# Kernel optimization log

Measured on AMD Instinct MI355X. Metric: run time of the kernel, lower is better.

## Reference

```python
import jax, jax.numpy as jnp
import numpy as np

EMBED_DIM = 1280
NUM_HEADS = 16
HEAD_DIM = EMBED_DIM // NUM_HEADS  # 80
SCALE = HEAD_DIM ** -0.5
BATCH = 16
SEQ = 1024


def setup_inputs() -> dict:
    key = jax.random.key(0)
    k1, k2, k3, k4, k5 = jax.random.split(key, 5)
    return {
        "hidden_states": jax.random.normal(k1, (BATCH, SEQ, EMBED_DIM), dtype=jnp.float32),
        "w_qkv": jax.random.normal(k2, (EMBED_DIM, 3 * EMBED_DIM), dtype=jnp.float32) * (EMBED_DIM ** -0.5),
        "b_qkv": jax.random.normal(k3, (3 * EMBED_DIM,), dtype=jnp.float32) * 0.02,
        "w_proj": jax.random.normal(k4, (EMBED_DIM, EMBED_DIM), dtype=jnp.float32) * (EMBED_DIM ** -0.5),
        "b_proj": jax.random.normal(k5, (EMBED_DIM,), dtype=jnp.float32) * 0.02,
    }


def reference(hidden_states, w_qkv, b_qkv, w_proj, b_proj):
    b, s, e = hidden_states.shape
    # QKV projection: [b, s, 3e] -> [3, b, h, s, d]
    qkv = hidden_states @ w_qkv + b_qkv
    qkv = qkv.reshape(b, s, 3, NUM_HEADS, HEAD_DIM).transpose(2, 0, 3, 1, 4)
    q, k, v = qkv[0], qkv[1], qkv[2]
    # full attention matrix [b, h, s, s]
    attn = jnp.einsum("bhqd,bhkd->bhqk", q, k) * SCALE
    attn = jax.nn.softmax(attn, axis=-1)
    # dropout p=0.0 (eval): identity
    out = jnp.einsum("bhqk,bhkd->bhqd", attn, v)
    out = out.transpose(0, 2, 1, 3).reshape(b, s, e)
    return out @ w_proj + b_proj
```

## Files before the change

### kernel.cpp

```cpp
#include <hip/hip_runtime.h>

#define BATCH 16
#define SEQ   1024
#define EMBED 1280
#define NH    16
#define HD    80
#define HDP   96
#define NQKV  3840
#define MTOK  (BATCH*SEQ)
#define SCALE 0.11180339887498948f
#define LOG2E 1.4426950408889634f

#define SK_STRIDE 104
#define SV_STRIDE 72
#define SP_STRIDE 72

typedef _Float16 half8 __attribute__((ext_vector_type(8)));
typedef _Float16 half4 __attribute__((ext_vector_type(4)));
typedef float floatx4 __attribute__((ext_vector_type(4)));

#define GLD_TO_LDS(gp, lp)                                                        \
  __builtin_amdgcn_global_load_lds(                                               \
      (const __attribute__((address_space(1))) void*)(gp),                        \
      (__attribute__((address_space(3))) void*)(lp), 16, 0, 0)

__device__ __forceinline__ float rowmax16(float x) {
#define DPP_MAX(ctrl)                                                             \
  {                                                                               \
    float y = __int_as_float(                                                     \
        __builtin_amdgcn_update_dpp(0, __float_as_int(x), ctrl, 0xF, 0xF, true)); \
    x = fmaxf(x, y);                                                              \
  }
  DPP_MAX(0xB1);
  DPP_MAX(0x4E);
  DPP_MAX(0x141);
  DPP_MAX(0x140);
#undef DPP_MAX
  return x;
}

__global__ void cvt_f32_to_f16(const float4* __restrict__ in, _Float16* __restrict__ out, int n4) {
  int i = blockIdx.x * blockDim.x + threadIdx.x;
  if (i < n4) {
    float4 v = in[i];
    half4 h;
    h[0] = (_Float16)v.x; h[1] = (_Float16)v.y; h[2] = (_Float16)v.z; h[3] = (_Float16)v.w;
    *(half4*)(out + (size_t)i * 4) = h;
  }
}

template <int N>
__global__ void cvt_transpose_f16(const float* __restrict__ in, _Float16* __restrict__ out) {
  __shared__ float tile[32][33];
  const int tx = threadIdx.x & 31, ty = threadIdx.x >> 5;
  const int k0 = blockIdx.y * 32;
  const int n0 = blockIdx.x * 32;
#pragma unroll
  for (int j = 0; j < 4; ++j)
    tile[ty + 8 * j][tx] = in[(size_t)(k0 + ty + 8 * j) * N + n0 + tx];
  __syncthreads();
#pragma unroll
  for (int j = 0; j < 4; ++j)
    out[(size_t)(n0 + ty + 8 * j) * 1280 + k0 + tx] = (_Float16)tile[tx][ty + 8 * j];
}

template <int MODE, int NT>
__global__ __launch_bounds__(256, 2)
void gemm_kernel(const _Float16* __restrict__ A, const _Float16* __restrict__ Bt,
                 const float* __restrict__ bias,
                 _Float16* __restrict__ q_pad, _Float16* __restrict__ k_pad,
                 _Float16* __restrict__ v_t, float* __restrict__ outf) {
  __shared__ __align__(16) _Float16 sA[2][128 * 32];
  __shared__ __align__(16) _Float16 sB[2][128 * 32];
  const int K = 1280;
  const int tid = threadIdx.x;
  const int wave = tid >> 6;
  const int lane = tid & 63;
  const int quad = lane >> 4;
  const int r16 = lane & 15;
  const int wm = wave >> 1, wn = wave & 1;

  const int pid = blockIdx.x;
  const int xcd = pid & 7;
  const int local = pid >> 3;
  const int panel = local / (8 * NT);
  const int rr = local - panel * (8 * NT);
  const int pm = rr & 7;
  const int pn = rr >> 3;
  const int m0 = (xcd * 16 + panel * 8 + pm) * 128;
  const int n0 = pn * 128;

  floatx4 acc[4][4] = {};

  const int c_base = wave * 128 + lane;

#define ISSUE(k0, buf)                                                              \
  do {                                                                              \
    _Pragma("unroll")                                                               \
    for (int i = 0; i < 2; ++i) {                                                   \
      int c = c_base + i * 64;                                                      \
      int row = c >> 2, kc = c & 3;                                                 \
      GLD_TO_LDS(A + (size_t)(m0 + row) * K + (k0) + kc * 8,                        \
                 &sA[buf][(wave * 2 + i) * 512]);                                   \
      GLD_TO_LDS(Bt + (size_t)(n0 + row) * K + (k0) + kc * 8,                       \
                 &sB[buf][(wave * 2 + i) * 512]);                                   \
    }                                                                               \
  } while (0)

  ISSUE(0, 0);
  for (int kt = 0; kt < 40; ++kt) {
    __syncthreads();
    if (kt + 1 < 40) ISSUE((kt + 1) * 32, (kt + 1) & 1);
    const _Float16* pA = sA[kt & 1];
    const _Float16* pB = sB[kt & 1];

    half8 af[4], bf[4];
#pragma unroll
    for (int mi = 0; mi < 4; ++mi)
      af[mi] = *(const half8*)(pA + (wm * 64 + mi * 16 + r16) * 32 + quad * 8);
#pragma unroll
    for (int ni = 0; ni < 4; ++ni)
      bf[ni] = *(const half8*)(pB + (wn * 64 + ni * 16 + r16) * 32 + quad * 8);
#pragma unroll
    for (int mi = 0; mi < 4; ++mi)
#pragma unroll
      for (int ni = 0; ni < 4; ++ni)
        acc[mi][ni] = __builtin_amdgcn_mfma_f32_16x16x32_f16(af[mi], bf[ni], acc[mi][ni], 0, 0, 0);
  }

  if (MODE == 1) {
#pragma unroll
    for (int mi = 0; mi < 4; ++mi)
#pragma unroll
      for (int ni = 0; ni < 4; ++ni) {
        int n = n0 + wn * 64 + ni * 16 + r16;
        float bv = bias[n];
#pragma unroll
        for (int r = 0; r < 4; ++r) {
          int m = m0 + wm * 64 + mi * 16 + quad * 4 + r;
          outf[(size_t)m * EMBED + n] = acc[mi][ni][r] + bv;
        }
      }
  } else {
#pragma unroll
    for (int mi = 0; mi < 4; ++mi)
#pragma unroll
      for (int ni = 0; ni < 4; ++ni) {
        int n = n0 + wn * 64 + ni * 16 + r16;
        float bv = bias[n];
        int which = n / 1280;
        int rem = n - which * 1280;
        int h = rem / 80;
        int d = rem - h * 80;
#pragma unroll
        for (int r = 0; r < 4; ++r) {
          int m = m0 + wm * 64 + mi * 16 + quad * 4 + r;
          int b = m >> 10, s = m & 1023;
          int bh = b * NH + h;
          _Float16 val = (_Float16)(acc[mi][ni][r] + bv);
          if (which == 0) {
            q_pad[((size_t)bh * SEQ + s) * HDP + d] = val;
            if (d < 16) q_pad[((size_t)bh * SEQ + s) * HDP + 80 + d] = (_Float16)0.f;
          } else if (which == 1) {
            k_pad[((size_t)bh * SEQ + s) * HDP + d] = val;
            if (d < 16) k_pad[((size_t)bh * SEQ + s) * HDP + 80 + d] = (_Float16)0.f;
          } else {
            v_t[((size_t)bh * HD + d) * SEQ + s] = val;
          }
        }
      }
  }
}

__global__ __launch_bounds__(256, 2)
void attn_kernel(const _Float16* __restrict__ q_pad, const _Float16* __restrict__ k_pad,
                 const _Float16* __restrict__ v_t, _Float16* __restrict__ attn_out) {
  __shared__ __align__(16) _Float16 sK[64 * SK_STRIDE];
  __shared__ __align__(16) _Float16 sV[96 * SV_STRIDE];
  __shared__ __align__(16) _Float16 sP[4][16 * SP_STRIDE];

  const int tid = threadIdx.x;
  const int wave = tid >> 6, lane = tid & 63, quad = lane >> 4, r16 = lane & 15;
  const int bh = blockIdx.x >> 3;
  const int q0 = (blockIdx.x & 7) * 128;

  if (tid < 128) {
    int row = 80 + (tid >> 3), col = (tid & 7) * 8;
    half8 z;
#pragma unroll
    for (int j = 0; j < 8; ++j) z[j] = (row == 80) ? (_Float16)1.f : (_Float16)0.f;
    *(half8*)(sV + row * SV_STRIDE + col) = z;
  }

  half8 qf[2][3];
#pragma unroll
  for (int mi = 0; mi < 2; ++mi) {
    const _Float16* qb = q_pad + ((size_t)bh * SEQ + q0 + wave * 32 + mi * 16 + r16) * HDP;
#pragma unroll
    for (int kq = 0; kq < 3; ++kq) {
      half8 q = *(const half8*)(qb + kq * 32 + quad * 8);
#pragma unroll
      for (int j = 0; j < 8; ++j) q[j] = q[j] * (_Float16)(SCALE * LOG2E);
      qf[mi][kq] = q;
    }
  }

  int rowK[3], colK[3];
#pragma unroll
  for (int i = 0; i < 3; ++i) {
    int c = tid + i * 256;
    rowK[i] = c / 12; colK[i] = c - rowK[i] * 12;
  }
  const int rowV0 = tid >> 3, colV0 = tid & 7;
  const _Float16* kgb = k_pad + ((size_t)bh * SEQ) * HDP;
  const _Float16* vgb = v_t + (size_t)bh * HD * SEQ;

  floatx4 o[2][6] = {};
  float mrow[2][4];
#pragma unroll
  for (int mi = 0; mi < 2; ++mi)
#pragma unroll
    for (int r = 0; r < 4; ++r) mrow[mi][r] = -1e30f;

  for (int kt = 0; kt < 16; ++kt) {
    __syncthreads();
    {
      uint4 tk0 = *(const uint4*)(kgb + ((size_t)(kt * 64 + rowK[0])) * HDP + colK[0] * 8);
      uint4 tk1 = *(const uint4*)(kgb + ((size_t)(kt * 64 + rowK[1])) * HDP + colK[1] * 8);
      uint4 tk2 = *(const uint4*)(kgb + ((size_t)(kt * 64 + rowK[2])) * HDP + colK[2] * 8);
      uint4 tv0 = *(const uint4*)(vgb + (size_t)(rowV0) * SEQ + kt * 64 + colV0 * 8);
      uint4 tv1 = *(const uint4*)(vgb + (size_t)(rowV0 + 32) * SEQ + kt * 64 + colV0 * 8);
      uint4 tv2;
      if (tid < 128)
        tv2 = *(const uint4*)(vgb + (size_t)(rowV0 + 64) * SEQ + kt * 64 + colV0 * 8);
      *(uint4*)(sK + rowK[0] * SK_STRIDE + colK[0] * 8) = tk0;
      *(uint4*)(sK + rowK[1] * SK_STRIDE + colK[1] * 8) = tk1;
      *(uint4*)(sK + rowK[2] * SK_STRIDE + colK[2] * 8) = tk2;
      *(uint4*)(sV + (rowV0) * SV_STRIDE + colV0 * 8) = tv0;
      *(uint4*)(sV + (rowV0 + 32) * SV_STRIDE + colV0 * 8) = tv1;
      if (tid < 128)
        *(uint4*)(sV + (rowV0 + 64) * SV_STRIDE + colV0 * 8) = tv2;
    }
    __syncthreads();

    floatx4 sacc[2][4] = {};
#pragma unroll
    for (int ni = 0; ni < 4; ++ni)
#pragma unroll
      for (int kq = 0; kq < 3; ++kq) {
        half8 kf = *(const half8*)(sK + (ni * 16 + r16) * SK_STRIDE + kq * 32 + quad * 8);
#pragma unroll
        for (int mi = 0; mi < 2; ++mi)
          sacc[mi][ni] = __builtin_amdgcn_mfma_f32_16x16x32_f16(qf[mi][kq], kf, sacc[mi][ni], 0, 0, 0);
      }

#pragma unroll
    for (int mi = 0; mi < 2; ++mi)
#pragma unroll
      for (int r = 0; r < 4; ++r) {
        float mx = fmaxf(fmaxf(sacc[mi][0][r], sacc[mi][1][r]),
                         fmaxf(sacc[mi][2][r], sacc[mi][3][r]));
        mx = rowmax16(mx);
        float mnew = fmaxf(mrow[mi][r], mx);
        float alpha = __builtin_amdgcn_exp2f(mrow[mi][r] - mnew);
        mrow[mi][r] = mnew;
#pragma unroll
        for (int ni = 0; ni < 4; ++ni)
          sacc[mi][ni][r] = __builtin_amdgcn_exp2f(sacc[mi][ni][r] - mnew);
#pragma unroll
        for (int di = 0; di < 6; ++di) o[mi][di][r] *= alpha;
      }

#pragma unroll
    for (int mi = 0; mi < 2; ++mi) {
#pragma unroll
      for (int ni = 0; ni < 4; ++ni)
#pragma unroll
        for (int r = 0; r < 4; ++r)
          sP[wave][(quad * 4 + r) * SP_STRIDE + ni * 16 + r16] = (_Float16)sacc[mi][ni][r];
#pragma unroll
      for (int kp = 0; kp < 2; ++kp) {
        half8 pf = *(const half8*)(&sP[wave][r16 * SP_STRIDE + kp * 32 + quad * 8]);
#pragma unroll
        for (int di = 0; di < 6; ++di) {
          half8 vf = *(const half8*)(sV + (di * 16 + r16) * SV_STRIDE + kp * 32 + quad * 8);
          o[mi][di] = __builtin_amdgcn_mfma_f32_16x16x32_f16(pf, vf, o[mi][di], 0, 0, 0);
        }
      }
    }
  }

  const int b = bh >> 4, h = bh & 15;
#pragma unroll
  for (int mi = 0; mi < 2; ++mi)
#pragma unroll
    for (int r = 0; r < 4; ++r) {
      float l = __shfl(o[mi][5][r], lane & 48);
      float inv = 1.0f / l;
      int tok = b * SEQ + q0 + wave * 32 + mi * 16 + quad * 4 + r;
#pragma unroll
      for (int di = 0; di < 5; ++di) {
        int e = h * HD + di * 16 + r16;
        attn_out[(size_t)tok * EMBED + e] = (_Float16)(o[mi][di][r] * inv);
      }
    }
}

extern "C" void kernel_launch(void* const* d_in, const int* in_sizes, int n_in,
                              void* d_out, int out_size, void* d_ws, size_t ws_size,
                              hipStream_t stream) {
  const float* hidden = (const float*)d_in[0];
  const float* w_qkv  = (const float*)d_in[1];
  const float* b_qkv  = (const float*)d_in[2];
  const float* w_proj = (const float*)d_in[3];
  const float* b_proj = (const float*)d_in[4];
  float* out = (float*)d_out;

  char* ws = (char*)d_ws;
  size_t off = 0;
  _Float16* hidden_h = (_Float16*)(ws + off); off += (size_t)MTOK * EMBED * 2;
  _Float16* wqkv_t   = (_Float16*)(ws + off); off += (size_t)NQKV * EMBED * 2;
  _Float16* wproj_t  = (_Float16*)(ws + off); off += (size_t)EMBED * EMBED * 2;
  _Float16* q_pad    = (_Float16*)(ws + off); off += (size_t)BATCH * NH * SEQ * HDP * 2;
  _Float16* k_pad    = (_Float16*)(ws + off); off += (size_t)BATCH * NH * SEQ * HDP * 2;
  _Float16* v_t      = (_Float16*)(ws + off); off += (size_t)BATCH * NH * HD * SEQ * 2;
  _Float16* attn_out = hidden_h;

  {
    int n4 = MTOK * EMBED / 4;
    cvt_f32_to_f16<<<(n4 + 255) / 256, 256, 0, stream>>>((const float4*)hidden, hidden_h, n4);
  }
  cvt_transpose_f16<NQKV><<<dim3(NQKV / 32, 1280 / 32), 256, 0, stream>>>(w_qkv, wqkv_t);
  cvt_transpose_f16<EMBED><<<dim3(EMBED / 32, 1280 / 32), 256, 0, stream>>>(w_proj, wproj_t);

  gemm_kernel<0, 30><<<128 * 30, 256, 0, stream>>>(
      hidden_h, wqkv_t, b_qkv, q_pad, k_pad, v_t, nullptr);

  attn_kernel<<<BATCH * NH * (SEQ / 128), 256, 0, stream>>>(q_pad, k_pad, v_t, attn_out);

  gemm_kernel<1, 10><<<128 * 10, 256, 0, stream>>>(
      attn_out, wproj_t, b_proj, nullptr, nullptr, nullptr, out);
}
```

Before: 677.8 us.

## Replace 128x128 GEMM with 256x256 8-wave pipelined GEMM with swizzled LDS

Both projection GEMMs move from a 128x128x32 tile with 4 waves to a 256x256x64 tile with 8 waves. Loads are staged in half-tiles and interleaved with MFMA quadrants under explicit barriers, s_setprio and vmcnt waits. The LDS layout uses an XOR swizzle to avoid bank conflicts. The larger tile raises data reuse per LDS byte, but it also increases LDS use (128KB) and register pressure, and it relies on hand-tuned waitcnt correctness.

```diff
diff --git a/kernel.cpp b/kernel.cpp
--- a/kernel.cpp
+++ b/kernel.cpp
@@ -64,86 +64,139 @@
     out[(size_t)(n0 + ty + 8 * j) * 1280 + k0 + tx] = (_Float16)tile[tx][ty + 8 * j];
 }
 
-template <int MODE, int NT>
-__global__ __launch_bounds__(256, 2)
-void gemm_kernel(const _Float16* __restrict__ A, const _Float16* __restrict__ Bt,
-                 const float* __restrict__ bias,
-                 _Float16* __restrict__ q_pad, _Float16* __restrict__ k_pad,
-                 _Float16* __restrict__ v_t, float* __restrict__ outf) {
-  __shared__ __align__(16) _Float16 sA[2][128 * 32];
-  __shared__ __align__(16) _Float16 sB[2][128 * 32];
-  const int K = 1280;
+
+#define STAGE_A(H, T, D)                                                           \
+  do {                                                                             \
+    GLD_TO_LDS(aSrc0 + (size_t)((H) * 128) * 1280 + (T) * 64,                      \
+               &sA[D][((H) * 128 + wave * 16) * 64]);                              \
+    GLD_TO_LDS(aSrc0 + (size_t)((H) * 128 + 8) * 1280 + (T) * 64,                  \
+               &sA[D][((H) * 128 + wave * 16 + 8) * 64]);                          \
+  } while (0)
+
+#define STAGE_B(H, T, D)                                                           \
+  do {                                                                             \
+    GLD_TO_LDS(bSrc0 + (size_t)((H) * 128) * 1280 + (T) * 64,                      \
+               &sB[D][((H) * 128 + wave * 16) * 64]);                              \
+    GLD_TO_LDS(bSrc0 + (size_t)((H) * 128 + 8) * 1280 + (T) * 64,                  \
+               &sB[D][((H) * 128 + wave * 16 + 8) * 64]);                          \
+  } while (0)
+
+#define LDS_FRAG(P, ROWB, FR, KK) (*(const half8*)((P) + ((ROWB) + (FR) * 16) * 64 + cofs[KK]))
+
+#define MFMA_Q(MIB, NIB)                                                           \
+  _Pragma("unroll") for (int mi = 0; mi < 4; ++mi)                                 \
+    _Pragma("unroll") for (int ni = 0; ni < 2; ++ni)                               \
+      _Pragma("unroll") for (int kk = 0; kk < 2; ++kk)                             \
+        acc[(MIB) + mi][(NIB) + ni] = __builtin_amdgcn_mfma_f32_16x16x32_f16(      \
+            af[mi][kk], bf[(NIB) + ni][kk], acc[(MIB) + mi][(NIB) + ni], 0, 0, 0)
+
+#define GBODY(T, D, S1, S2, VNSTR)                                                 \
+  {                                                                                \
+    const _Float16* pA = &sA[D][0];                                                \
+    const _Float16* pB = &sB[D][0];                                                \
+                         \
+    _Pragma("unroll") for (int mi = 0; mi < 4; ++mi)                               \
+      _Pragma("unroll") for (int kk = 0; kk < 2; ++kk)                             \
+        af[mi][kk] = LDS_FRAG(pA, rA, mi, kk);                                     \
+    _Pragma("unroll") for (int ni = 0; ni < 2; ++ni)                               \
+      _Pragma("unroll") for (int kk = 0; kk < 2; ++kk)                             \
+        bf[ni][kk] = LDS_FRAG(pB, rB, ni, kk);                                     \
+    if (S1) { STAGE_A(1, (T) + 1, (D) ^ 1); }                                      \
+    __builtin_amdgcn_s_barrier();                                                  \
+    asm volatile("s_waitcnt lgkmcnt(0)" ::: "memory");                             \
+    __builtin_amdgcn_s_setprio(1);                                                 \
+    MFMA_Q(0, 0);                                                                  \
+    __builtin_amdgcn_s_setprio(0);                                                 \
+    __builtin_amdgcn_s_barrier();                                                  \
+                                                   \
+    _Pragma("unroll") for (int ni = 0; ni < 2; ++ni)                               \
+      _Pragma("unroll") for (int kk = 0; kk < 2; ++kk)                             \
+        bf[2 + ni][kk] = LDS_FRAG(pB, rB, 2 + ni, kk);                             \
+    __builtin_amdgcn_s_barrier();                                                  \
+    asm volatile("s_waitcnt lgkmcnt(0)" ::: "memory");                             \
+    __builtin_amdgcn_s_setprio(1);                                                 \
+    MFMA_Q(0, 2);                                                                  \
+    __builtin_amdgcn_s_setprio(0);                                                 \
+    __builtin_amdgcn_s_barrier();                                                  \
+                                  \
+    _Pragma("unroll") for (int mi = 0; mi < 4; ++mi)                               \
+      _Pragma("unroll") for (int kk = 0; kk < 2; ++kk)                             \
+        af[mi][kk] = LDS_FRAG(pA, rA, 4 + mi, kk);                                 \
+    if (S2) { STAGE_B(0, (T) + 2, (D)); }                                          \
+    __builtin_amdgcn_s_barrier();                                                  \
+    asm volatile("s_waitcnt lgkmcnt(0)" ::: "memory");                             \
+    __builtin_amdgcn_s_setprio(1);                                                 \
+    MFMA_Q(4, 0);                                                                  \
+    __builtin_amdgcn_s_setprio(0);                                                 \
+    __builtin_amdgcn_s_barrier();                                                  \
+            \
+    if (S2) { STAGE_A(0, (T) + 2, (D)); STAGE_B(1, (T) + 2, (D)); }                \
+    __builtin_amdgcn_s_barrier();                                                  \
+    __builtin_amdgcn_s_setprio(1);                                                 \
+    MFMA_Q(4, 2);                                                                  \
+    __builtin_amdgcn_s_setprio(0);                                                 \
+    asm volatile("s_waitcnt " VNSTR ::: "memory");                                 \
+    __builtin_amdgcn_s_barrier();                                                  \
+  }
+
+template <int MODE>
+__global__ __launch_bounds__(512, 2)
+void gemm256(const _Float16* __restrict__ A, const _Float16* __restrict__ Bt,
+             const float* __restrict__ bias,
+             _Float16* __restrict__ q_pad, _Float16* __restrict__ k_pad,
+             _Float16* __restrict__ v_t, float* __restrict__ outf) {
+  __shared__ __align__(16) _Float16 sA[2][256 * 64];
+  __shared__ __align__(16) _Float16 sB[2][256 * 64];
+
   const int tid = threadIdx.x;
-  const int wave = tid >> 6;
-  const int lane = tid & 63;
-  const int quad = lane >> 4;
-  const int r16 = lane & 15;
-  const int wm = wave >> 1, wn = wave & 1;
+  const int wave = tid >> 6, lane = tid & 63, quad = lane >> 4, r16 = lane & 15;
+  const int wm = wave >> 2, wn = wave & 3;
 
   const int pid = blockIdx.x;
-  const int xcd = pid & 7;
-  const int local = pid >> 3;
-  const int panel = local / (8 * NT);
-  const int rr = local - panel * (8 * NT);
-  const int pm = rr & 7;
-  const int pn = rr >> 3;
-  const int m0 = (xcd * 16 + panel * 8 + pm) * 128;
-  const int n0 = pn * 128;
-
-  floatx4 acc[4][4] = {};
-
-  const int c_base = wave * 128 + lane;
-
-#define ISSUE(k0, buf)                                                              \
-  do {                                                                              \
-    _Pragma("unroll")                                                               \
-    for (int i = 0; i < 2; ++i) {                                                   \
-      int c = c_base + i * 64;                                                      \
-      int row = c >> 2, kc = c & 3;                                                 \
-      GLD_TO_LDS(A + (size_t)(m0 + row) * K + (k0) + kc * 8,                        \
-                 &sA[buf][(wave * 2 + i) * 512]);                                   \
-      GLD_TO_LDS(Bt + (size_t)(n0 + row) * K + (k0) + kc * 8,                       \
-                 &sB[buf][(wave * 2 + i) * 512]);                                   \
-    }                                                                               \
-  } while (0)
-
-  ISSUE(0, 0);
-  for (int kt = 0; kt < 40; ++kt) {
-    __syncthreads();
-    if (kt + 1 < 40) ISSUE((kt + 1) * 32, (kt + 1) & 1);
-    const _Float16* pA = sA[kt & 1];
-    const _Float16* pB = sB[kt & 1];
-
-    half8 af[4], bf[4];
-#pragma unroll
-    for (int mi = 0; mi < 4; ++mi)
-      af[mi] = *(const half8*)(pA + (wm * 64 + mi * 16 + r16) * 32 + quad * 8);
-#pragma unroll
-    for (int ni = 0; ni < 4; ++ni)
-      bf[ni] = *(const half8*)(pB + (wn * 64 + ni * 16 + r16) * 32 + quad * 8);
-#pragma unroll
-    for (int mi = 0; mi < 4; ++mi)
-#pragma unroll
-      for (int ni = 0; ni < 4; ++ni)
-        acc[mi][ni] = __builtin_amdgcn_mfma_f32_16x16x32_f16(af[mi], bf[ni], acc[mi][ni], 0, 0, 0);
-  }
+  const int xcd = pid & 7, local = pid >> 3;
+  const int mt = xcd * 8 + (local & 7);
+  const int nt = local >> 3;
+  const int m0 = mt * 256, n0 = nt * 256;
+
+  const int l8 = lane >> 3, cg = (lane & 7) ^ l8;
+  const _Float16* aSrc0 = A + ((size_t)m0 + wave * 16 + l8) * 1280 + cg * 8;
+  const _Float16* bSrc0 = Bt + ((size_t)n0 + wave * 16 + l8) * 1280 + cg * 8;
+
+  const int rA = wm * 128 + r16;
+  const int rB = wn * 64 + r16;
+  const int cofs[2] = { ((0 + quad) ^ (r16 & 7)) * 8, ((4 + quad) ^ (r16 & 7)) * 8 };
+
+  floatx4 acc[8][4] = {};
+  half8 af[4][2], bf[4][2];
+
+  STAGE_A(0, 0, 0); STAGE_A(1, 0, 0); STAGE_B(0, 0, 0); STAGE_B(1, 0, 0);
+  STAGE_B(0, 1, 1); STAGE_A(0, 1, 1); STAGE_B(1, 1, 1);
+  asm volatile("s_waitcnt vmcnt(6)" ::: "memory");
+  __builtin_amdgcn_s_barrier();
+
+  for (int it = 0; it < 9; ++it) {
+    GBODY(2 * it, 0, true, true, "vmcnt(6)");
+    GBODY(2 * it + 1, 1, true, true, "vmcnt(6)");
+  }
+  GBODY(18, 0, true, false, "vmcnt(0)");
+  GBODY(19, 1, false, false, "vmcnt(0)");
 
   if (MODE == 1) {
 #pragma unroll
-    for (int mi = 0; mi < 4; ++mi)
+    for (int mi = 0; mi < 8; ++mi)
 #pragma unroll
       for (int ni = 0; ni < 4; ++ni) {
         int n = n0 + wn * 64 + ni * 16 + r16;
         float bv = bias[n];
 #pragma unroll
         for (int r = 0; r < 4; ++r) {
-          int m = m0 + wm * 64 + mi * 16 + quad * 4 + r;
+          int m = m0 + wm * 128 + mi * 16 + quad * 4 + r;
           outf[(size_t)m * EMBED + n] = acc[mi][ni][r] + bv;
         }
       }
   } else {
 #pragma unroll
-    for (int mi = 0; mi < 4; ++mi)
+    for (int mi = 0; mi < 8; ++mi)
 #pragma unroll
       for (int ni = 0; ni < 4; ++ni) {
         int n = n0 + wn * 64 + ni * 16 + r16;
@@ -154,7 +207,7 @@
         int d = rem - h * 80;
 #pragma unroll
         for (int r = 0; r < 4; ++r) {
-          int m = m0 + wm * 64 + mi * 16 + quad * 4 + r;
+          int m = m0 + wm * 128 + mi * 16 + quad * 4 + r;
           int b = m >> 10, s = m & 1023;
           int bh = b * NH + h;
           _Float16 val = (_Float16)(acc[mi][ni][r] + bv);
@@ -333,11 +386,9 @@
   cvt_transpose_f16<NQKV><<<dim3(NQKV / 32, 1280 / 32), 256, 0, stream>>>(w_qkv, wqkv_t);
   cvt_transpose_f16<EMBED><<<dim3(EMBED / 32, 1280 / 32), 256, 0, stream>>>(w_proj, wproj_t);
 
-  gemm_kernel<0, 30><<<128 * 30, 256, 0, stream>>>(
-      hidden_h, wqkv_t, b_qkv, q_pad, k_pad, v_t, nullptr);
+  gemm256<0><<<960, 512, 0, stream>>>(hidden_h, wqkv_t, b_qkv, q_pad, k_pad, v_t, nullptr);
 
   attn_kernel<<<BATCH * NH * (SEQ / 128), 256, 0, stream>>>(q_pad, k_pad, v_t, attn_out);
 
-  gemm_kernel<1, 10><<<128 * 10, 256, 0, stream>>>(
-      attn_out, wproj_t, b_proj, nullptr, nullptr, nullptr, out);
-}
+  gemm256<1><<<320, 512, 0, stream>>>(attn_out, wproj_t, b_proj, nullptr, nullptr, nullptr, out);
+}
```

After: 650.3 us. 4.1% less time.
